# Kernel optimization log

Measured on AMD Instinct MI355X. Metric: run time of the kernel, lower is better.

## Reference

```python
import jax, jax.numpy as jnp
import numpy as np

# DETR-style matcher constants
COST_CLASS, COST_BBOX, COST_GIOU = 1.0, 5.0, 2.0
BS, Q, NUM_CLASSES, T = 16, 900, 92, 100  # 16 images, 900 queries, 100 targets/image


def setup_inputs() -> dict:
    key = jax.random.key(0)
    k1, k2, k3, k4, k5, k6 = jax.random.split(key, 6)
    pred_logits = jax.random.normal(k1, (BS, Q, NUM_CLASSES), dtype=jnp.float32)
    # predicted boxes in cxcywh, valid sizes
    cxcy = jax.random.uniform(k2, (BS, Q, 2), dtype=jnp.float32)
    wh = jax.random.uniform(k3, (BS, Q, 2), dtype=jnp.float32) * 0.5 + 0.01
    pred_boxes = jnp.concatenate([cxcy, wh], axis=-1)
    # targets: ids and xyxy boxes, concatenated over the batch (T per image)
    tgt_ids = jax.random.randint(k4, (BS * T,), 0, NUM_CLASSES, dtype=jnp.int64)
    tc = jax.random.uniform(k5, (BS * T, 2), dtype=jnp.float32)
    tw = jax.random.uniform(k6, (BS * T, 2), dtype=jnp.float32) * 0.5 + 0.01
    tgt_bbox = jnp.concatenate([tc - tw / 2.0, tc + tw / 2.0], axis=-1)  # xyxy
    return {"pred_logits": pred_logits, "pred_boxes": pred_boxes,
            "tgt_ids": tgt_ids, "tgt_bbox": tgt_bbox}


def box_cxcywh_to_xyxy(b):
    c, s = b[..., :2], b[..., 2:]
    return jnp.concatenate([c - s / 2.0, c + s / 2.0], axis=-1)


def box_xyxy_to_cxcywh(b):
    return jnp.concatenate([(b[..., :2] + b[..., 2:]) / 2.0,
                            b[..., 2:] - b[..., :2]], axis=-1)


def generalized_box_iou(a, b):
    # a: [N,4] xyxy, b: [M,4] xyxy -> [N,M]
    area_a = (a[:, 2] - a[:, 0]) * (a[:, 3] - a[:, 1])
    area_b = (b[:, 2] - b[:, 0]) * (b[:, 3] - b[:, 1])
    lt = jnp.maximum(a[:, None, :2], b[None, :, :2])
    rb = jnp.minimum(a[:, None, 2:], b[None, :, 2:])
    wh = jnp.clip(rb - lt, 0.0)
    inter = wh[..., 0] * wh[..., 1]
    union = area_a[:, None] + area_b[None, :] - inter
    iou = inter / union
    lt_c = jnp.minimum(a[:, None, :2], b[None, :, :2])
    rb_c = jnp.maximum(a[:, None, 2:], b[None, :, 2:])
    wh_c = jnp.clip(rb_c - lt_c, 0.0)
    area_c = wh_c[..., 0] * wh_c[..., 1]
    return iou - (area_c - union) / area_c


def _cost_matrix(pred_logits, pred_boxes, tgt_ids, tgt_bbox):
    bs, q, nc = pred_logits.shape
    out_prob = jax.nn.softmax(pred_logits.reshape(-1, nc), axis=-1)  # [bs*Q, C]
    out_bbox = pred_boxes.reshape(-1, 4)                              # [bs*Q, 4] cxcywh
    cost_class = -out_prob[:, tgt_ids]                                # [bs*Q, M]
    cost_bbox = jnp.abs(out_bbox[:, None, :] -
                        box_xyxy_to_cxcywh(tgt_bbox)[None, :, :]).sum(-1)  # L1 cdist
    cost_giou = -generalized_box_iou(box_cxcywh_to_xyxy(out_bbox), tgt_bbox)
    C = COST_BBOX * cost_bbox + COST_CLASS * cost_class + COST_GIOU * cost_giou
    return C.reshape(bs, q, -1)


_cost_matrix_jit = jax.jit(_cost_matrix)


def _lsa(cost):
    # Jonker-Volgenant shortest augmenting path; cost [n, m] with n <= m.
    # Returns col assignment for each row (minimizing total cost).
    n, m = cost.shape
    u = np.zeros(n + 1)
    v = np.zeros(m + 1)
    p = np.zeros(m + 1, dtype=np.int64)   # p[j] = row (1-indexed) assigned to col j
    way = np.zeros(m + 1, dtype=np.int64)
    cpad = np.zeros((n + 1, m + 1))
    cpad[1:, 1:] = cost
    for i in range(1, n + 1):
        p[0] = i
        j0 = 0
        minv = np.full(m + 1, np.inf)
        used = np.zeros(m + 1, dtype=bool)
        while True:
            used[j0] = True
            i0 = p[j0]
            idx = np.nonzero(~used)[0]
            idx = idx[idx > 0]
            cur = cpad[i0, idx] - u[i0] - v[idx]
            better = cur < minv[idx]
            minv[idx[better]] = cur[better]
            way[idx[better]] = j0
            k = np.argmin(minv[idx])
            delta = minv[idx[k]]
            j1 = idx[k]
            u[p[used]] += delta
            v[used] -= delta
            minv[~used] -= delta
            j0 = j1
            if p[j0] == 0:
                break
        while j0:
            j1 = way[j0]
            p[j0] = p[j1]
            j0 = j1
    ans = np.zeros(n, dtype=np.int64)
    for j in range(1, m + 1):
        if p[j] > 0:
            ans[p[j] - 1] = j - 1
    return ans


def reference(pred_logits, pred_boxes, tgt_ids, tgt_bbox):
    C = _cost_matrix_jit(pred_logits, pred_boxes, tgt_ids, tgt_bbox)  # [BS, Q, BS*T]
    Cn = np.asarray(C)
    rows = np.zeros((BS, T), dtype=np.int64)
    cols = np.zeros((BS, T), dtype=np.int64)
    for i in range(BS):  # per-image serial assignment, as in the original
        c = Cn[i, :, i * T:(i + 1) * T]          # [Q, T], Q >= T
        pred_for_tgt = _lsa(c.T)                 # [T]: target j -> query row
        order = np.argsort(pred_for_tgt)         # scipy returns sorted row indices
        rows[i] = pred_for_tgt[order]
        cols[i] = order
    return C, jnp.asarray(rows), jnp.asarray(cols)
```

## Files before the change

### kernel.cpp

```cpp
#include <hip/hip_runtime.h>
#include <math.h>

#define BS 16
#define QN 900
#define NC 92
#define TN 100
#define NQ (BS * QN)
#define NT (BS * TN)
#define C_ELEMS ((size_t)NQ * NT)
#define NK 15
#define F4N 225
#define NS 16
#define ARR_CAP 300
#define UNM_CAP 416

__device__ __forceinline__ unsigned f32_sortable(float f) {
    unsigned u = __float_as_uint(f);
    return (u & 0x80000000u) ? ~u : (u | 0x80000000u);
}
__device__ __forceinline__ float f32_unsortable(unsigned s) {
    return __uint_as_float((s & 0x80000000u) ? (s ^ 0x80000000u) : ~s);
}

template<int CTRL>
__device__ __forceinline__ float dpp_fmin_step(float x) {
    int xi = __float_as_int(x);
    int yi = __builtin_amdgcn_update_dpp(xi, xi, CTRL, 0xF, 0xF, false);
    return fminf(x, __int_as_float(yi));
}
__device__ __forceinline__ float wave_fmin_to63(float x) {
    x = dpp_fmin_step<0x111>(x);
    x = dpp_fmin_step<0x112>(x);
    x = dpp_fmin_step<0x114>(x);
    x = dpp_fmin_step<0x118>(x);
    x = dpp_fmin_step<0x142>(x);
    x = dpp_fmin_step<0x143>(x);
    return x;
}
__device__ __forceinline__ float readlane63_f(float x) {
    return __uint_as_float(__builtin_amdgcn_readlane(__float_as_uint(x), 63));
}

__device__ __forceinline__ int slot_of(int c) { return ((c >> 8) << 2) | (c & 3); }
__device__ __forceinline__ int owner_of(int c) { return (c >> 2) & 63; }

__device__ __forceinline__ int read_colreg16(const int arr[NS], int c) {
    int s = slot_of(c);
    int v = 0;
    #pragma unroll
    for (int k = 0; k < NS; ++k) if (k == s) v = arr[k];
    return __builtin_amdgcn_readlane(v, owner_of(c));
}

__device__ __forceinline__ float readrow_u(float u0, float u1, int r) {
    return __uint_as_float(__builtin_amdgcn_readlane(
        __float_as_uint(r < 64 ? u0 : u1), r & 63));
}

__device__ __forceinline__ void issue_row(const float4* cst4, int irow, int lane,
        float4& r0, float4& r1, float4& r2, float4& r3) {
    const float4* cr = cst4 + (size_t)(irow - 1) * F4N;
    r0 = cr[lane];
    r1 = cr[lane + 64];
    r2 = cr[lane + 128];
    if (lane < 33) r3 = cr[lane + 192];
}

__device__ __forceinline__ float cost_entry(
        float px2, float py2, float pw, float ph,
        float ax0, float ay0, float ax1, float ay1,
        float area_a, float base_cls, float4 tb) {
    float tw = tb.z - tb.x;
    float th = tb.w - tb.y;
    float area_b = tw * th;
    float sx = px2 - (tb.x + tb.z);
    float sy = py2 - (tb.y + tb.w);
    float dw = pw - tw;
    float dh = ph - th;
    float cb = fmaf(0.5f, fabsf(sx), fabsf(dw)) + fmaf(0.5f, fabsf(sy), fabsf(dh));
    float ltx = fmaxf(ax0, tb.x), lty = fmaxf(ay0, tb.y);
    float rbx = fminf(ax1, tb.z), rby = fminf(ay1, tb.w);
    float iw = fmaxf(rbx - ltx, 0.0f), ih = fmaxf(rby - lty, 0.0f);
    float inter = iw * ih;
    float uni = (area_a + area_b) - inter;
    float cx0 = fminf(ax0, tb.x), cy0 = fminf(ay0, tb.y);
    float cx1 = fmaxf(ax1, tb.z), cy1 = fmaxf(ay1, tb.w);
    float area_c = (cx1 - cx0) * (cy1 - cy0);
    float num = fmaf(uni, uni, inter * area_c);
    float r   = __builtin_amdgcn_rcpf(uni * area_c);
    return fmaf(-2.0f, num * r, fmaf(5.0f, cb, base_cls));
}

__global__ __launch_bounds__(256) void softmax_cost_kernel(
        const float* __restrict__ logits,
        const float4* __restrict__ pboxes,
        const int4* __restrict__ tids4,
        const float4* __restrict__ tbox,
        float* __restrict__ C,
        unsigned long long* __restrict__ rm) {
    if (blockIdx.x < 7) {
        int idx = blockIdx.x * 256 + threadIdx.x;
        if (idx < NT) rm[idx] = ~0ull;
    }
    __shared__ float shp[4][NC];
    int wid = threadIdx.x >> 6;
    int lane = threadIdx.x & 63;
    int q = blockIdx.x * 4 + wid;
    const float* row = logits + (size_t)q * NC;
    float x0 = (lane < NC) ? row[lane] : -INFINITY;
    float x1 = (lane + 64 < NC) ? row[lane + 64] : -INFINITY;
    float m = fmaxf(x0, x1);
    for (int off = 32; off; off >>= 1) m = fmaxf(m, __shfl_xor(m, off));
    float e0 = (lane < NC) ? expf(x0 - m) : 0.0f;
    float e1 = (lane + 64 < NC) ? expf(x1 - m) : 0.0f;
    float s = e0 + e1;
    for (int off = 32; off; off >>= 1) s += __shfl_xor(s, off);
    float rs = __builtin_amdgcn_rcpf(s);
    if (lane < NC) shp[wid][lane] = fmaf(-e0, rs, 2.0f);
    if (lane + 64 < NC) shp[wid][lane + 64] = fmaf(-e1, rs, 2.0f);
    __syncthreads();
    float4 pb = pboxes[q];
    float hx = pb.z * 0.5f, hy = pb.w * 0.5f;
    float ax0 = pb.x - hx, ay0 = pb.y - hy;
    float ax1 = pb.x + hx, ay1 = pb.y + hy;
    float area_a = pb.z * pb.w;
    float px2 = pb.x + pb.x, py2 = pb.y + pb.y;
    float4* crow4 = (float4*)(C + (size_t)q * NT);
    for (int t4 = lane; t4 < NT / 4; t4 += 64) {
        int4 id = tids4[t4];
        int t = t4 * 4;
        float4 r;
        r.x = cost_entry(px2, py2, pb.z, pb.w, ax0, ay0, ax1, ay1, area_a,
                         shp[wid][id.x], tbox[t]);
        r.y = cost_entry(px2, py2, pb.z, pb.w, ax0, ay0, ax1, ay1, area_a,
                         shp[wid][id.y], tbox[t + 1]);
        r.z = cost_entry(px2, py2, pb.z, pb.w, ax0, ay0, ax1, ay1, area_a,
                         shp[wid][id.z], tbox[t + 2]);
        r.w = cost_entry(px2, py2, pb.z, pb.w, ax0, ay0, ax1, ay1, area_a,
                         shp[wid][id.w], tbox[t + 3]);
        crow4[t4] = r;
    }
}

__global__ __launch_bounds__(256) void diag_transpose_kernel(
        const float* __restrict__ C, float* __restrict__ cost_t,
        unsigned long long* __restrict__ rm) {
    __shared__ float tile[64][65];
    int b = blockIdx.x;
    int q0 = blockIdx.y * 64;
    int t0 = blockIdx.z * 64;
    int tx = threadIdx.x & 63;
    int ty = threadIdx.x >> 6;
    for (int r = ty; r < 64; r += 4) {
        int q = q0 + r, t = t0 + tx;
        if (q < QN && t < TN)
            tile[r][tx] = C[(size_t)(b * QN + q) * NT + b * TN + t];
    }
    __syncthreads();
    for (int r = ty; r < 64; r += 4) {
        int t = t0 + r, q = q0 + tx;
        if (q < QN && t < TN)
            cost_t[(size_t)(b * TN + t) * QN + q] = tile[tx][r];
    }
    if (threadIdx.x < 64) {
        int t = t0 + threadIdx.x;
        if (t < TN) {
            int qmax = min(64, QN - q0);
            float mv = INFINITY; int ma = 0;
            for (int r = 0; r < qmax; ++r) {
                float x = tile[r][threadIdx.x];
                if (x < mv) { mv = x; ma = q0 + r; }
            }
            unsigned long long key =
                ((unsigned long long)f32_sortable(mv) << 20) | (unsigned)ma;
            atomicMin(&rm[b * TN + t], key);
        }
    }
}

__global__ __launch_bounds__(64, 1) void lsa_kernel(
        const float* __restrict__ cost_t,
        const unsigned long long* __restrict__ rm,
        float* __restrict__ out) {
    int b = blockIdx.x;
    int lane = threadIdx.x;
    const float4* cst4 = (const float4*)(cost_t + (size_t)b * TN * QN);
    __shared__ float u_s[TN];
    __shared__ int p_s[QN];
    __shared__ int unm[UNM_CAP];
    __shared__ int dij[128];

    float v_r[NS], dist_r[NS];
    int way_r[NS], pcol_r[NS];
    float4 pre0, pre1, pre2, pre3 = make_float4(0.f, 0.f, 0.f, 0.f);
    float4 rc0, rc1, rc2, rc3 = make_float4(0.f, 0.f, 0.f, 0.f);
    const bool v3 = (lane < 33);

    #pragma unroll
    for (int s = 0; s < NS; ++s) v_r[s] = 0.0f;
    for (int j = lane; j < QN; j += 64) p_s[j] = 0x7fffffff;
    int arg0 = 0, arg1 = 0;
    float u0 = 0.0f, u1 = 0.0f;
    {
        unsigned long long kk = rm[b * TN + lane];
        u0 = f32_unsortable((unsigned)(kk >> 20));
        arg0 = (int)(kk & 0xFFFFFu);
        u_s[lane] = u0;
        if (lane + 64 < TN) {
            unsigned long long k1 = rm[b * TN + lane + 64];
            u1 = f32_unsortable((unsigned)(k1 >> 20));
            arg1 = (int)(k1 & 0xFFFFFu);
            u_s[lane + 64] = u1;
        }
    }
    atomicMin(&p_s[arg0], lane + 1);
    if (lane + 64 < TN) atomicMin(&p_s[arg1], lane + 65);
    int nunm = 0;
    {
        bool um0 = (p_s[arg0] != lane + 1);
        unsigned long long m0 = __ballot(um0);
        if (um0) unm[__popcll(m0 & ((1ull << lane) - 1ull))] = lane + 1;
        nunm = __popcll(m0);
        bool um1 = (lane + 64 < TN) && (p_s[arg1] != lane + 65);
        unsigned long long m1 = __ballot(um1);
        if (um1) unm[nunm + __popcll(m1 & ((1ull << lane) - 1ull))] = lane + 65;
        nunm += __popcll(m1);
    }
    #pragma unroll
    for (int s = 0; s < NS; ++s) {
        int f = lane + ((s >> 2) << 6);
        int c = (f << 2) | (s & 3);
        pcol_r[s] = 0;
        if (f < F4N) { int pv = p_s[c]; pcol_r[s] = (pv == 0x7fffffff) ? 0 : pv; }
    }

    int qhead = 0, qtail = nunm, dij_n = 0, pops = 0;
    if (qhead < qtail) issue_row(cst4, unm[0], lane, pre0, pre1, pre2, pre3);
    while (qhead < qtail) {
        int i_cur = unm[qhead++];
        ++pops;
        if (pops > ARR_CAP) {
            if (lane == 0) dij[dij_n] = i_cur;
            dij_n++;
            continue;
        }
        float dd[NS];
        dd[0]  = pre0.x - v_r[0];  dd[1]  = pre0.y - v_r[1];
        dd[2]  = pre0.z - v_r[2];  dd[3]  = pre0.w - v_r[3];
        dd[4]  = pre1.x - v_r[4];  dd[5]  = pre1.y - v_r[5];
        dd[6]  = pre1.z - v_r[6];  dd[7]  = pre1.w - v_r[7];
        dd[8]  = pre2.x - v_r[8];  dd[9]  = pre2.y - v_r[9];
        dd[10] = pre2.z - v_r[10]; dd[11] = pre2.w - v_r[11];
        if (v3) {
            dd[12] = pre3.x - v_r[12]; dd[13] = pre3.y - v_r[13];
            dd[14] = pre3.z - v_r[14]; dd[15] = pre3.w - v_r[15];
        } else {
            dd[12] = INFINITY; dd[13] = INFINITY;
            dd[14] = INFINITY; dd[15] = INFINITY;
        }
        bool pf = false;
        if (qhead < qtail) { issue_row(cst4, unm[qhead], lane, pre0, pre1, pre2, pre3); pf = true; }
        float l1 = INFINITY, l2 = INFINITY; int ls = 0;
        #pragma unroll
        for (int s = 0; s < NS; ++s) {
            float d = dd[s];
            bool lt = d < l1;
            l2 = lt ? l1 : fminf(l2, d);
            ls = lt ? s : ls;
            l1 = lt ? d : l1;
        }
        float d1 = readlane63_f(wave_fmin_to63(l1));
        unsigned long long eqm = __ballot(l1 == d1);
        int wl = __ffsll(eqm) - 1;
        float cand2 = (lane == wl) ? l2 : l1;
        float d2 = readlane63_f(wave_fmin_to63(cand2));
        int myj = (lane << 2) + ((ls >> 2) << 8) + (ls & 3);
        int j1 = __builtin_amdgcn_readlane(myj, wl);
        int i0 = read_colreg16(pcol_r, j1);
        bool take = (d1 < d2) || (i0 == 0);
        if (take) {
            int s1 = slot_of(j1), ow = owner_of(j1);
            float dv_ = d2 - d1;
            #pragma unroll
            for (int s = 0; s < NS; ++s)
                if (s == s1 && lane == ow) { v_r[s] -= dv_; pcol_r[s] = i_cur; }
            if (lane == 0) {
                u_s[i_cur - 1] = d2;
                if (i0 != 0) unm[qtail] = i0;
            }
            if (i0 != 0) qtail++;
        } else {
            if (lane == 0) { u_s[i_cur - 1] = d2; dij[dij_n] = i_cur; }
            dij_n++;
        }
        if (!pf && qhead < qtail)
            issue_row(cst4, unm[qhead], lane, pre0, pre1, pre2, pre3);
    }
    u0 = u_s[lane];
    if (lane + 64 < TN) u1 = u_s[lane + 64];

    if (dij_n > 0) issue_row(cst4, dij[0], lane, pre0, pre1, pre2, pre3);

    for (int ui = 0; ui < dij_n; ++ui) {
        int i_cur = dij[ui];
        unsigned used_mask = 0;
        float uic = readrow_u(u0, u1, i_cur - 1);
        #pragma unroll
        for (int s = 0; s < NS; ++s) way_r[s] = -1;
        dist_r[0]  = (pre0.x - uic) - v_r[0];
        dist_r[1]  = (pre0.y - uic) - v_r[1];
        dist_r[2]  = (pre0.z - uic) - v_r[2];
        dist_r[3]  = (pre0.w - uic) - v_r[3];
        dist_r[4]  = (pre1.x - uic) - v_r[4];
        dist_r[5]  = (pre1.y - uic) - v_r[5];
        dist_r[6]  = (pre1.z - uic) - v_r[6];
        dist_r[7]  = (pre1.w - uic) - v_r[7];
        dist_r[8]  = (pre2.x - uic) - v_r[8];
        dist_r[9]  = (pre2.y - uic) - v_r[9];
        dist_r[10] = (pre2.z - uic) - v_r[10];
        dist_r[11] = (pre2.w - uic) - v_r[11];
        if (v3) {
            dist_r[12] = (pre3.x - uic) - v_r[12];
            dist_r[13] = (pre3.y - uic) - v_r[13];
            dist_r[14] = (pre3.z - uic) - v_r[14];
            dist_r[15] = (pre3.w - uic) - v_r[15];
        } else {
            dist_r[12] = INFINITY; dist_r[13] = INFINITY;
            dist_r[14] = INFINITY; dist_r[15] = INFINITY;
        }
        if (ui + 1 < dij_n) issue_row(cst4, dij[ui + 1], lane, pre0, pre1, pre2, pre3);

        float dfin; int jfree;
        while (true) {
            float dv[NS]; int dk[NS];
            #pragma unroll
            for (int s = 0; s < NS; ++s) {
                dv[s] = (used_mask & (1u << s)) ? INFINITY : dist_r[s];
                dk[s] = s;
            }
            #pragma unroll
            for (int n = 8; n >= 1; n >>= 1) {
                #pragma unroll
                for (int i = 0; i < n; ++i) {
                    bool tk = dv[2 * i + 1] < dv[2 * i];
                    dv[i] = tk ? dv[2 * i + 1] : dv[2 * i];
                    dk[i] = tk ? dk[2 * i + 1] : dk[2 * i];
                }
            }
            float lv = dv[0];
            int s0 = dk[0];
            int li = (lane << 2) + ((s0 >> 2) << 8) + (s0 & 3);
            float dmin = readlane63_f(wave_fmin_to63(lv));
            unsigned long long eq = __ballot(lv == dmin);
            int winner = __ffsll(eq) - 1;
            int j1 = __builtin_amdgcn_readlane(li, winner);
            int pj1 = read_colreg16(pcol_r, j1);
            if (pj1 == 0) { dfin = dmin; jfree = j1; break; }
            {
                int s1 = slot_of(j1), ow1 = owner_of(j1);
                if (lane == ow1) used_mask |= (1u << s1);
            }
            issue_row(cst4, pj1, lane, rc0, rc1, rc2, rc3);
            float ui0 = readrow_u(u0, u1, pj1 - 1);
            float off = dmin - ui0;
            #define RELAX(S, V) \
                if (!(used_mask & (1u << (S)))) { \
                    float nd = ((V) - v_r[S]) + off; \
                    if (nd < dist_r[S]) { dist_r[S] = nd; way_r[S] = j1; } }
            RELAX(0,  rc0.x) RELAX(1,  rc0.y) RELAX(2,  rc0.z) RELAX(3,  rc0.w)
            RELAX(4,  rc1.x) RELAX(5,  rc1.y) RELAX(6,  rc1.z) RELAX(7,  rc1.w)
            RELAX(8,  rc2.x) RELAX(9,  rc2.y) RELAX(10, rc2.z) RELAX(11, rc2.w)
            if (v3) {
                RELAX(12, rc3.x) RELAX(13, rc3.y) RELAX(14, rc3.z) RELAX(15, rc3.w)
            }
            #undef RELAX
        }
        #pragma unroll
        for (int s = 0; s < NS; ++s) {
            if (used_mask & (1u << s)) {
                float a = dfin - dist_r[s];
                v_r[s] -= a;
                u_s[pcol_r[s] - 1] += a;
            }
        }
        if (lane == 0) u_s[i_cur - 1] += dfin;
        u0 = u_s[lane];
        if (lane + 64 < TN) u1 = u_s[lane + 64];
        {
            int jj = jfree;
            while (true) {
                int wj = read_colreg16(way_r, jj);
                int pn = (wj < 0) ? i_cur : read_colreg16(pcol_r, wj);
                int sj = slot_of(jj), ow = owner_of(jj);
                #pragma unroll
                for (int s = 0; s < NS; ++s)
                    if (s == sj && lane == ow) pcol_r[s] = pn;
                if (wj < 0) break;
                jj = wj;
            }
        }
    }

    #pragma unroll
    for (int s = 0; s < NS; ++s) {
        int f = lane + ((s >> 2) << 6);
        int c = (f << 2) | (s & 3);
        if (f < F4N) p_s[c] = pcol_r[s];
    }
    float* rows = out + C_ELEMS + (size_t)b * TN;
    float* cols = out + C_ELEMS + (size_t)BS * TN + (size_t)b * TN;
    int base = 0;
    #pragma unroll
    for (int k = 0; k < NK; ++k) {
        int c = lane + (k << 6);
        int pv = (c < QN) ? p_s[c] : 0;
        unsigned long long mask = __ballot(pv > 0);
        if (pv > 0) {
            int rank = base + __popcll(mask & ((1ull << lane) - 1ull));
            rows[rank] = (float)c;
            cols[rank] = (float)(pv - 1);
        }
        base += __popcll(mask);
    }
}

extern "C" void kernel_launch(void* const* d_in, const int* in_sizes, int n_in,
                              void* d_out, int out_size, void* d_ws, size_t ws_size,
                              hipStream_t stream) {
    const float* logits = (const float*)d_in[0];
    const float4* pboxes = (const float4*)d_in[1];
    const int* tids = (const int*)d_in[2];
    const float4* tbox = (const float4*)d_in[3];
    float* out = (float*)d_out;

    float* cost_t = (float*)d_ws;
    unsigned long long* rm =
        (unsigned long long*)(cost_t + (size_t)BS * TN * QN);

    softmax_cost_kernel<<<NQ / 4, 256, 0, stream>>>(logits, pboxes, (const int4*)tids, tbox, out, rm);
    diag_transpose_kernel<<<dim3(BS, 15, 2), 256, 0, stream>>>(out, cost_t, rm);
    lsa_kernel<<<BS, 64, 0, stream>>>(cost_t, rm, out);
}
```

Baseline: 176.6 us.

## Fuse diagonal transpose into cost kernel and compute column minima inside LSA

```diff
diff --git a/kernel.cpp b/kernel.cpp
--- a/kernel.cpp
+++ b/kernel.cpp
@@ -13,14 +13,6 @@
 #define NS 16
 #define ARR_CAP 300
 #define UNM_CAP 416
-
-__device__ __forceinline__ unsigned f32_sortable(float f) {
-    unsigned u = __float_as_uint(f);
-    return (u & 0x80000000u) ? ~u : (u | 0x80000000u);
-}
-__device__ __forceinline__ float f32_unsortable(unsigned s) {
-    return __uint_as_float((s & 0x80000000u) ? (s ^ 0x80000000u) : ~s);
-}
 
 template<int CTRL>
 __device__ __forceinline__ float dpp_fmin_step(float x) {
@@ -97,11 +89,7 @@
         const int4* __restrict__ tids4,
         const float4* __restrict__ tbox,
         float* __restrict__ C,
-        unsigned long long* __restrict__ rm) {
-    if (blockIdx.x < 7) {
-        int idx = blockIdx.x * 256 + threadIdx.x;
-        if (idx < NT) rm[idx] = ~0ull;
-    }
+        float* __restrict__ cost_t) {
     __shared__ float shp[4][NC];
     int wid = threadIdx.x >> 6;
     int lane = threadIdx.x & 63;
@@ -125,7 +113,11 @@
     float ax1 = pb.x + hx, ay1 = pb.y + hy;
     float area_a = pb.z * pb.w;
     float px2 = pb.x + pb.x, py2 = pb.y + pb.y;
+    int b = q / QN;
+    int diag_lo = b * 25;
+    float* ctb = cost_t + (size_t)b * TN * QN + (q - b * QN);
     float4* crow4 = (float4*)(C + (size_t)q * NT);
+    #pragma unroll 2
     for (int t4 = lane; t4 < NT / 4; t4 += 64) {
         int4 id = tids4[t4];
         int t = t4 * 4;
@@ -139,48 +131,19 @@
         r.w = cost_entry(px2, py2, pb.z, pb.w, ax0, ay0, ax1, ay1, area_a,
                          shp[wid][id.w], tbox[t + 3]);
         crow4[t4] = r;
-    }
-}
-
-__global__ __launch_bounds__(256) void diag_transpose_kernel(
-        const float* __restrict__ C, float* __restrict__ cost_t,
-        unsigned long long* __restrict__ rm) {
-    __shared__ float tile[64][65];
-    int b = blockIdx.x;
-    int q0 = blockIdx.y * 64;
-    int t0 = blockIdx.z * 64;
-    int tx = threadIdx.x & 63;
-    int ty = threadIdx.x >> 6;
-    for (int r = ty; r < 64; r += 4) {
-        int q = q0 + r, t = t0 + tx;
-        if (q < QN && t < TN)
-            tile[r][tx] = C[(size_t)(b * QN + q) * NT + b * TN + t];
-    }
-    __syncthreads();
-    for (int r = ty; r < 64; r += 4) {
-        int t = t0 + r, q = q0 + tx;
-        if (q < QN && t < TN)
-            cost_t[(size_t)(b * TN + t) * QN + q] = tile[tx][r];
-    }
-    if (threadIdx.x < 64) {
-        int t = t0 + threadIdx.x;
-        if (t < TN) {
-            int qmax = min(64, QN - q0);
-            float mv = INFINITY; int ma = 0;
-            for (int r = 0; r < qmax; ++r) {
-                float x = tile[r][threadIdx.x];
-                if (x < mv) { mv = x; ma = q0 + r; }
-            }
-            unsigned long long key =
-                ((unsigned long long)f32_sortable(mv) << 20) | (unsigned)ma;
-            atomicMin(&rm[b * TN + t], key);
+        int tl = t4 - diag_lo;
+        if ((unsigned)tl < 25u) {
+            float* dst = ctb + (size_t)(4 * tl) * QN;
+            dst[0]        = r.x;
+            dst[QN]       = r.y;
+            dst[2 * QN]   = r.z;
+            dst[3 * QN]   = r.w;
         }
     }
 }
 
 __global__ __launch_bounds__(64, 1) void lsa_kernel(
         const float* __restrict__ cost_t,
-        const unsigned long long* __restrict__ rm,
         float* __restrict__ out) {
     int b = blockIdx.x;
     int lane = threadIdx.x;
@@ -188,7 +151,7 @@
     __shared__ float u_s[TN];
     __shared__ int p_s[QN];
     __shared__ int unm[UNM_CAP];
-    __shared__ int dij[128];
+    __shared__ int dij[UNM_CAP];
 
     float v_r[NS], dist_r[NS];
     int way_r[NS], pcol_r[NS];
@@ -199,20 +162,42 @@
     #pragma unroll
     for (int s = 0; s < NS; ++s) v_r[s] = 0.0f;
     for (int j = lane; j < QN; j += 64) p_s[j] = 0x7fffffff;
+
     int arg0 = 0, arg1 = 0;
     float u0 = 0.0f, u1 = 0.0f;
     {
-        unsigned long long kk = rm[b * TN + lane];
-        u0 = f32_unsortable((unsigned)(kk >> 20));
-        arg0 = (int)(kk & 0xFFFFFu);
-        u_s[lane] = u0;
-        if (lane + 64 < TN) {
-            unsigned long long k1 = rm[b * TN + lane + 64];
-            u1 = f32_unsortable((unsigned)(k1 >> 20));
-            arg1 = (int)(k1 & 0xFFFFFu);
-            u_s[lane + 64] = u1;
-        }
-    }
+        float4 s0, s1, s2, s3 = make_float4(0.f, 0.f, 0.f, 0.f);
+        issue_row(cst4, 1, lane, s0, s1, s2, s3);
+        for (int tt = 0; tt < TN; ++tt) {
+            float4 c0 = s0, c1 = s1, c2 = s2, c3 = s3;
+            if (tt + 1 < TN) issue_row(cst4, tt + 2, lane, s0, s1, s2, s3);
+            float dd[NS];
+            dd[0]  = c0.x; dd[1]  = c0.y; dd[2]  = c0.z; dd[3]  = c0.w;
+            dd[4]  = c1.x; dd[5]  = c1.y; dd[6]  = c1.z; dd[7]  = c1.w;
+            dd[8]  = c2.x; dd[9]  = c2.y; dd[10] = c2.z; dd[11] = c2.w;
+            if (v3) { dd[12] = c3.x; dd[13] = c3.y; dd[14] = c3.z; dd[15] = c3.w; }
+            else    { dd[12] = INFINITY; dd[13] = INFINITY;
+                      dd[14] = INFINITY; dd[15] = INFINITY; }
+            float l1 = INFINITY; int ls = 0;
+            #pragma unroll
+            for (int s = 0; s < NS; ++s) {
+                bool lt = dd[s] < l1;
+                ls = lt ? s : ls;
+                l1 = lt ? dd[s] : l1;
+            }
+            float mv = readlane63_f(wave_fmin_to63(l1));
+            unsigned long long eq = __ballot(l1 == mv);
+            int wl = __ffsll(eq) - 1;
+            int myq = (lane << 2) + ((ls >> 2) << 8) + (ls & 3);
+            int ma = __builtin_amdgcn_readlane(myq, wl);
+            if (lane == (tt & 63)) {
+                if (tt < 64) { u0 = mv; arg0 = ma; }
+                else         { u1 = mv; arg1 = ma; }
+            }
+            if (lane == 0) u_s[tt] = mv;
+        }
+    }
+
     atomicMin(&p_s[arg0], lane + 1);
     if (lane + 64 < TN) atomicMin(&p_s[arg1], lane + 65);
     int nunm = 0;
@@ -434,10 +419,7 @@
     float* out = (float*)d_out;
 
     float* cost_t = (float*)d_ws;
-    unsigned long long* rm =
-        (unsigned long long*)(cost_t + (size_t)BS * TN * QN);
-
-    softmax_cost_kernel<<<NQ / 4, 256, 0, stream>>>(logits, pboxes, (const int4*)tids, tbox, out, rm);
-    diag_transpose_kernel<<<dim3(BS, 15, 2), 256, 0, stream>>>(out, cost_t, rm);
-    lsa_kernel<<<BS, 64, 0, stream>>>(cost_t, rm, out);
-}
+
+    softmax_cost_kernel<<<NQ / 4, 256, 0, stream>>>(logits, pboxes, (const int4*)tids, tbox, out, cost_t);
+    lsa_kernel<<<BS, 64, 0, stream>>>(cost_t, out);
+}
```

Measured after the change: 204.2 us. +15.7%, slower.
